# Optimization experiments

Measured on AMD Instinct MI355X. Metric: run time of the kernel, lower is better.

## Reference

```python
import jax, jax.numpy as jnp
import numpy as np

P_SCALAR = 40.0
NEG_INF = -1e30


def setup_inputs() -> dict:
    key = jax.random.key(0)
    k1, k2, k3, k4, k5 = jax.random.split(key, 5)
    B, Dk, Dv, T, H, W = 8, 128, 512, 2, 56, 56
    qkey = jax.random.normal(k1, (B, Dk, H, W), dtype=jnp.float32)
    qmask = jax.random.randint(k2, (B, 1, H, W), 0, 2).astype(jnp.bool_)
    mkey = jax.random.normal(k3, (B, Dk, T, H, W), dtype=jnp.float32)
    mval = jax.random.normal(k4, (B, Dv, T, H, W), dtype=jnp.float32)
    mmask = jax.random.randint(k5, (B, 1, T, H, W), 0, 2).astype(jnp.bool_)
    return {"qkey": qkey, "qmask": qmask, "mkey": mkey, "mval": mval, "mmask": mmask}


def reference(qkey, qmask, mkey, mval, mmask):
    # Faithful vectorized version of SegmentationAttentionSeparateModule.maskRead.
    # Torch loops over b, gathers masked query/memory columns, does
    # softmax(p_scalar * mk^T qk, dim=0) then mv @ p, scattering into zeros.
    # Equivalent dense math: masked softmax over memory positions, and zero
    # output at query positions outside qmask.
    B, Dk, H, W = qkey.shape
    Dv = mval.shape[1]
    M = H * W                       # query positions
    qk = qkey.reshape(B, Dk, M)     # [B, Dk, M]
    mk = mkey.reshape(B, Dk, -1)    # [B, Dk, N], N = T*H*W
    mv = mval.reshape(B, Dv, -1)    # [B, Dv, N]
    qm = qmask.reshape(B, 1, M)     # [B, 1, M]
    mm = mmask.reshape(B, -1)       # [B, N]

    # scores over memory (axis 1) per query column, p_scalar * mk^T qk
    scores = P_SCALAR * jnp.einsum('bdn,bdm->bnm', mk, qk)       # [B, N, M]
    scores = jnp.where(mm[:, :, None], scores, NEG_INF)
    p = jax.nn.softmax(scores, axis=1)                           # softmax over memory
    p = jnp.where(mm[:, :, None], p, 0.0)                        # guard all-masked rows
    qread = jnp.einsum('bdn,bnm->bdm', mv, p)                    # [B, Dv, M]
    qread = jnp.where(qm, qread, 0.0)                            # only masked query cols
    return qread.reshape(B, Dv, H, W)
```

## Files before the change

kernel.cpp:

```cpp
#include <hip/hip_runtime.h>
#include <stdint.h>

#define B_    8
#define DK_   128
#define DV_   512
#define M_    3136
#define N_    6272
#define MT128_ 25
#define NSEG_ 8
#define NTILES_ 98
#define TH_   30.0f
#define MARGIN_ 36.0f
#define BKT_  64

typedef short bf16x8 __attribute__((ext_vector_type(8)));
typedef float f32x16 __attribute__((ext_vector_type(16)));
typedef unsigned short u16x8 __attribute__((ext_vector_type(8)));

__device__ __forceinline__ unsigned fkey(float x) {
  unsigned u = __float_as_uint(x);
  return (u & 0x80000000u) ? ~u : (u | 0x80000000u);
}
__device__ __forceinline__ float fdec(unsigned k) {
  return __uint_as_float((k & 0x80000000u) ? (k & 0x7fffffffu) : ~k);
}
__device__ __forceinline__ unsigned short f2bf(float x) {
  unsigned u = __float_as_uint(x);
  return (unsigned short)((u + 0x7fffu + ((u >> 16) & 1u)) >> 16);
}
__device__ __forceinline__ float bf2f(unsigned short h) {
  return __uint_as_float(((unsigned)h) << 16);
}

__global__ __launch_bounds__(256)
void prep_kernel(const float* __restrict__ qkey, const int* __restrict__ qmask,
                 const float* __restrict__ mkey, const float* __restrict__ mval,
                 float* __restrict__ qkeyT, unsigned short* __restrict__ qkb,
                 float* __restrict__ mkeyT, unsigned short* __restrict__ mkb,
                 unsigned short* __restrict__ mvalT,
                 int* __restrict__ qlist, int* __restrict__ qcnt,
                 unsigned* __restrict__ zbase) {
  __shared__ float T[64][65];
  int r = blockIdx.x;
  int lane = threadIdx.x & 63, ri = threadIdx.x >> 6;
  if (r < 784) {
    int xt = r % 49, dt = (r / 49) & 1, b = r / 98;
    #pragma unroll
    for (int k = 0; k < 16; ++k) {
      int dl = ri * 16 + k;
      T[dl][lane] = qkey[((size_t)b * DK_ + dt * 64 + dl) * M_ + xt * 64 + lane];
    }
    __syncthreads();
    #pragma unroll
    for (int k = 0; k < 16; ++k) {
      int xl = ri * 16 + k;
      float v = 40.0f * T[lane][xl];
      size_t idx = ((size_t)b * M_ + xt * 64 + xl) * DK_ + dt * 64 + lane;
      qkeyT[idx] = v;
      qkb[idx] = f2bf(v);
    }
  } else if (r < 2352) {
    int r2 = r - 784;
    int xt = r2 % 98, dt = (r2 / 98) & 1, b = r2 / 196;
    #pragma unroll
    for (int k = 0; k < 16; ++k) {
      int dl = ri * 16 + k;
      T[dl][lane] = mkey[((size_t)b * DK_ + dt * 64 + dl) * N_ + xt * 64 + lane];
    }
    __syncthreads();
    #pragma unroll
    for (int k = 0; k < 16; ++k) {
      int xl = ri * 16 + k;
      float v = T[lane][xl];
      size_t idx = ((size_t)b * N_ + xt * 64 + xl) * DK_ + dt * 64 + lane;
      mkeyT[idx] = v;
      mkb[idx] = f2bf(v);
    }
  } else if (r < 8624) {
    int r3 = r - 2352;
    int nt = r3 % 98, dvt = (r3 / 98) & 7, b = r3 / 784;
    #pragma unroll
    for (int k = 0; k < 16; ++k) {
      int dvl = ri * 16 + k;
      T[dvl][lane] = mval[((size_t)b * DV_ + dvt * 64 + dvl) * N_ + nt * 64 + lane];
    }
    __syncthreads();
    #pragma unroll
    for (int k = 0; k < 16; ++k) {
      int nl = ri * 16 + k;
      mvalT[((size_t)b * N_ + nt * 64 + nl) * DV_ + dvt * 64 + lane] = f2bf(T[lane][nl]);
    }
  } else if (r < 8632) {
    int b = r - 8624;
    __shared__ int wsum[4];
    __shared__ int cbase;
    int tid = threadIdx.x, wv = tid >> 6;
    if (tid == 0) cbase = 0;
    __syncthreads();
    for (int base = 0; base < M_; base += 256) {
      int i = base + tid;
      int flag = (i < M_) ? (qmask[b * M_ + i] != 0) : 0;
      unsigned long long bal = __ballot(flag);
      int prefix = __popcll(bal & ((1ull << lane) - 1ull));
      if (lane == 0) wsum[wv] = __popcll(bal);
      __syncthreads();
      int woff = 0;
      for (int t = 0; t < wv; ++t) woff += wsum[t];
      int total = wsum[0] + wsum[1] + wsum[2] + wsum[3];
      if (flag) qlist[b * M_ + cbase + woff + prefix] = i;
      __syncthreads();
      if (tid == 0) cbase += total;
      __syncthreads();
    }
    if (tid == 0) qcnt[b] = cbase;
  } else {
    int z = r - 8632;
    unsigned* p = zbase + z * 1024;
    for (int i = threadIdx.x; i < 1024; i += 256) p[i] = 0u;
  }
}

__global__ __launch_bounds__(256, 4)
void score_mfma(const unsigned short* __restrict__ qkb, const unsigned short* __restrict__ mkb,
                const int* __restrict__ qlist, const int* __restrict__ qcnt,
                const int* __restrict__ mmask,
                unsigned* __restrict__ maxkey, unsigned* __restrict__ bcnt,
                unsigned* __restrict__ bucket) {
  int bid = blockIdx.x;
  int seg = bid & (NSEG_ - 1);
  int t   = bid >> 3;
  int mt  = t % MT128_;
  int b   = t / MT128_;
  int mc = qcnt[b];
  if (mt * 128 >= mc) return;
  int t0 = (NTILES_ * seg) / NSEG_;
  int t1 = (NTILES_ * (seg + 1)) / NSEG_;

  __shared__ unsigned short Ks[2][64 * 128];

  int tid = threadIdx.x;
  int lane = tid & 63, wv = tid >> 6;
  int l31 = lane & 31, lhi = lane >> 5;
  int mrow = wv * 32 + l31;

  int cm = mt * 128 + mrow;
  int col = (cm < mc) ? qlist[b * M_ + cm] : qlist[b * M_];
  int mo  = (cm < mc) ? col : -1;
  const unsigned short* qrow = qkb + ((size_t)b * M_ + col) * DK_;
  bf16x8 qf[8];
  #pragma unroll
  for (int kc = 0; kc < 8; ++kc)
    qf[kc] = *(const bf16x8*)(qrow + (kc * 2 + lhi) * 8);

  const unsigned short* mkb_b = mkb + (size_t)b * N_ * DK_;
  const int* mm_b = mmask + b * N_;

  {
    int nbase = t0 << 6;
    char* kd = (char*)&Ks[0][0];
    #pragma unroll
    for (int i = 0; i < 4; ++i) {
      int c = wv * 4 + i;
      const unsigned short* src = mkb_b + ((size_t)(nbase + lane)) * DK_ + c * 8;
      __builtin_amdgcn_global_load_lds(
          (const __attribute__((address_space(1))) unsigned*)src,
          (__attribute__((address_space(3))) unsigned*)(kd + c * 1024), 16, 0, 0);
    }
  }
  asm volatile("s_waitcnt vmcnt(0)" ::: "memory");
  __syncthreads();

  float runmax = -3.0e38f;

  for (int tt = t0; tt < t1; ++tt) {
    int cur = (tt - t0) & 1;
    int nbase = tt << 6;
    if (tt + 1 < t1) {
      int nb2 = (tt + 1) << 6;
      char* kd = (char*)&Ks[cur ^ 1][0];
      #pragma unroll
      for (int i = 0; i < 4; ++i) {
        int c = wv * 4 + i;
        const unsigned short* src = mkb_b + ((size_t)(nb2 + lane)) * DK_ + c * 8;
        __builtin_amdgcn_global_load_lds(
            (const __attribute__((address_space(1))) unsigned*)src,
            (__attribute__((address_space(3))) unsigned*)(kd + c * 1024), 16, 0, 0);
      }
    }
    unsigned long long bits = __ballot(mm_b[nbase + lane] != 0);

    const char* kb = (const char*)&Ks[cur][0];
    f32x16 acc0, acc1;
    #pragma unroll
    for (int r = 0; r < 16; ++r) { acc0[r] = 0.f; acc1[r] = 0.f; }
    #pragma unroll
    for (int kc = 0; kc < 8; ++kc) {
      int c = kc * 2 + lhi;
      bf16x8 a0 = *(const bf16x8*)(kb + c * 1024 + l31 * 16);
      bf16x8 a1 = *(const bf16x8*)(kb + c * 1024 + (32 + l31) * 16);
      acc0 = __builtin_amdgcn_mfma_f32_32x32x16_bf16(a0, qf[kc], acc0, 0, 0, 0);
      acc1 = __builtin_amdgcn_mfma_f32_32x32x16_bf16(a1, qf[kc], acc1, 0, 0, 0);
    }

    unsigned long long b0 = bits >> (lhi << 2);
    unsigned long long b1 = (bits >> 32) >> (lhi << 2);
    float cmx = -3.0e38f;
    #pragma unroll
    for (int r = 0; r < 16; ++r) {
      const int pos = (r & 3) + ((r >> 2) << 3);
      if ((b0 >> pos) & 1) cmx = fmaxf(cmx, acc0[r]);
      if ((b1 >> pos) & 1) cmx = fmaxf(cmx, acc1[r]);
    }
    cmx = fmaxf(cmx, __shfl_xor(cmx, 32));
    runmax = fmaxf(runmax, cmx);

    unsigned old = 0u;
    if (lhi == 0 && mo >= 0) old = atomicMax(&maxkey[b * M_ + mo], fkey(runmax));

    if (mo >= 0) {
      float thr = runmax - MARGIN_;
      #pragma unroll
      for (int r = 0; r < 16; ++r) {
        const int pos = (r & 3) + ((r >> 2) << 3);
        if (((b0 >> pos) & 1) && acc0[r] >= thr) {
          unsigned slot = atomicAdd(&bcnt[b * M_ + mo], 1u);
          if (slot < (unsigned)BKT_)
            bucket[(((size_t)(b * M_ + mo)) << 6) + slot] =
                (unsigned)(nbase + pos + (lhi << 2));
        }
        if (((b1 >> pos) & 1) && acc1[r] >= thr) {
          unsigned slot = atomicAdd(&bcnt[b * M_ + mo], 1u);
          if (slot < (unsigned)BKT_)
            bucket[(((size_t)(b * M_ + mo)) << 6) + slot] =
                (unsigned)(nbase + 32 + pos + (lhi << 2));
        }
      }
    }
    if (lhi == 0) runmax = fmaxf(runmax, fdec(old));
    runmax = __shfl(runmax, l31);

    asm volatile("s_waitcnt vmcnt(0)" ::: "memory");
    __syncthreads();
  }
}

__device__ __forceinline__ float dot128(const float* __restrict__ q,
                                        const float* __restrict__ k) {
  float s = 0.f;
  #pragma unroll 8
  for (int i = 0; i < DK_; i += 4) {
    float4 a = *(const float4*)&q[i];
    float4 bb = *(const float4*)&k[i];
    s += a.x * bb.x + a.y * bb.y + a.z * bb.z + a.w * bb.w;
  }
  return s;
}

__global__ __launch_bounds__(256)
void pv_exact(const float* __restrict__ qkeyT, const float* __restrict__ mkeyT,
              const unsigned short* __restrict__ mvalT,
              const int* __restrict__ qlist, const int* __restrict__ qcnt,
              const int* __restrict__ mmask,
              const unsigned* __restrict__ bcnt, const unsigned* __restrict__ bucket,
              unsigned short* __restrict__ outT) {
  int b = blockIdx.y;
  int wv = threadIdx.x >> 6, lane = threadIdx.x & 63;
  int c = blockIdx.x * 4 + wv;
  if (c >= qcnt[b]) return;
  int m = qlist[b * M_ + c];
  unsigned cnt = bcnt[b * M_ + m];
  const float* qrow = qkeyT + ((size_t)b * M_ + m) * DK_;
  float acc[8] = {0.f, 0.f, 0.f, 0.f, 0.f, 0.f, 0.f, 0.f};
  float lsum = 0.f;

  if (cnt <= (unsigned)BKT_) {
    int n = -1;
    if (lane < (int)cnt) n = (int)bucket[(((size_t)(b * M_ + m)) << 6) + lane];
    float sv = -3.0e38f;
    if (n >= 0) sv = dot128(qrow, mkeyT + ((size_t)b * N_ + n) * DK_);
    float mx = sv;
    #pragma unroll
    for (int o = 32; o > 0; o >>= 1) mx = fmaxf(mx, __shfl_xor(mx, o));
    float e = (n >= 0 && sv >= mx - TH_) ? expf(sv - mx) : 0.f;
    lsum = e;
    #pragma unroll
    for (int o = 32; o > 0; o >>= 1) lsum += __shfl_xor(lsum, o);
    unsigned long long alive = __ballot(e > 0.f);
    while (alive) {
      int lb = __ffsll((unsigned long long)alive) - 1;
      alive &= alive - 1;
      float w = __shfl(e, lb);
      int nn = __shfl(n, lb);
      u16x8 vvv = *(const u16x8*)(mvalT + ((size_t)b * N_ + nn) * DV_ + lane * 8);
      #pragma unroll
      for (int r = 0; r < 8; ++r) acc[r] += w * bf2f(vvv[r]);
    }
  } else {
    float mx = -3.0e38f;
    for (int base = 0; base < N_; base += 64) {
      int n = base + lane;
      float sv = -3.0e38f;
      if (mmask[b * N_ + n] != 0)
        sv = dot128(qrow, mkeyT + ((size_t)b * N_ + n) * DK_);
      mx = fmaxf(mx, sv);
    }
    #pragma unroll
    for (int o = 32; o > 0; o >>= 1) mx = fmaxf(mx, __shfl_xor(mx, o));
    for (int base = 0; base < N_; base += 64) {
      int n = base + lane;
      bool act = (mmask[b * N_ + n] != 0);
      float sv = -3.0e38f;
      if (act) sv = dot128(qrow, mkeyT + ((size_t)b * N_ + n) * DK_);
      float e = (act && sv >= mx - TH_) ? expf(sv - mx) : 0.f;
      lsum += e;
      unsigned long long alive = __ballot(e > 0.f);
      while (alive) {
        int lb = __ffsll((unsigned long long)alive) - 1;
        alive &= alive - 1;
        float w = __shfl(e, lb);
        int nn = __shfl(n, lb);
        u16x8 vvv = *(const u16x8*)(mvalT + ((size_t)b * N_ + nn) * DV_ + lane * 8);
        #pragma unroll
        for (int r = 0; r < 8; ++r) acc[r] += w * bf2f(vvv[r]);
      }
    }
    #pragma unroll
    for (int o = 32; o > 0; o >>= 1) lsum += __shfl_xor(lsum, o);
  }

  float inv = (lsum > 0.f) ? 1.0f / lsum : 0.0f;
  u16x8 ov;
  #pragma unroll
  for (int r = 0; r < 8; ++r) ov[r] = f2bf(acc[r] * inv);
  *(u16x8*)(outT + ((size_t)b * M_ + m) * DV_ + lane * 8) = ov;
}

__global__ __launch_bounds__(256)
void finalize_T(const unsigned short* __restrict__ outT, const int* __restrict__ qmask,
                float* __restrict__ out) {
  __shared__ float T[64][65];
  int b = blockIdx.z, dvt = blockIdx.y, mt = blockIdx.x;
  int lane = threadIdx.x & 63, ri = threadIdx.x >> 6;
  #pragma unroll
  for (int k = 0; k < 16; ++k) {
    int ml = ri * 16 + k;
    int m = mt * 64 + ml;
    bool act = (qmask[b * M_ + m] != 0);
    T[ml][lane] = act ? bf2f(outT[((size_t)b * M_ + m) * DV_ + dvt * 64 + lane]) : 0.f;
  }
  __syncthreads();
  #pragma unroll
  for (int k = 0; k < 16; ++k) {
    int dvl = ri * 16 + k;
    out[((size_t)b * DV_ + dvt * 64 + dvl) * M_ + mt * 64 + lane] = T[lane][dvl];
  }
}

extern "C" void kernel_launch(void* const* d_in, const int* in_sizes, int n_in,
                              void* d_out, int out_size, void* d_ws, size_t ws_size,
                              hipStream_t stream) {
  const float* qkey  = (const float*)d_in[0];
  const int*   qmask = (const int*)d_in[1];
  const float* mkey  = (const float*)d_in[2];
  const float* mval  = (const float*)d_in[3];
  const int*   mmask = (const int*)d_in[4];
  float* out = (float*)d_out;

  uint8_t* w = (uint8_t*)d_ws;
  unsigned*       maxkey = (unsigned*)(w + 0);
  unsigned*       bcnt   = (unsigned*)(w + 100352);
  int*            qcnt   = (int*)(w + 200704);
  int*            qlist  = (int*)(w + 200832);
  unsigned*       bucket = (unsigned*)(w + 301184);
  float*          qkeyT  = (float*)(w + 6723712);
  float*          mkeyT  = (float*)(w + 19568768);
  unsigned short* qkb    = (unsigned short*)(w + 45258880);
  unsigned short* mkb    = (unsigned short*)(w + 51681408);
  unsigned short* outTb  = (unsigned short*)(w + 64526464);
  unsigned short* mvalT  = (unsigned short*)(w + 90216576);

  prep_kernel<<<8681, 256, 0, stream>>>(qkey, qmask, mkey, mval,
                                        qkeyT, qkb, mkeyT, mkb, mvalT,
                                        qlist, qcnt, maxkey );

  score_mfma<<<B_ * MT128_ * NSEG_, 256, 0, stream>>>(
      qkb, mkb, qlist, qcnt, mmask, maxkey, bcnt, bucket);

  pv_exact<<<dim3(M_ / 4, B_), 256, 0, stream>>>(
      qkeyT, mkeyT, mvalT, qlist, qcnt, mmask, bcnt, bucket, outTb);

  finalize_T<<<dim3(M_ / 64, DV_ / 64, B_), 256, 0, stream>>>(outTb, qmask, out);
}
```

Baseline: 186.8 us.

## Drop cross-segment max sharing, widen buckets, vectorize prep transposes, precompute mask bits

```diff
diff --git a/kernel.cpp b/kernel.cpp
--- a/kernel.cpp
+++ b/kernel.cpp
@@ -7,23 +7,16 @@
 #define M_    3136
 #define N_    6272
 #define MT128_ 25
-#define NSEG_ 8
+#define NSEG_ 16
 #define NTILES_ 98
 #define TH_   30.0f
 #define MARGIN_ 36.0f
-#define BKT_  64
+#define BKT_  128
 
 typedef short bf16x8 __attribute__((ext_vector_type(8)));
 typedef float f32x16 __attribute__((ext_vector_type(16)));
 typedef unsigned short u16x8 __attribute__((ext_vector_type(8)));
 
-__device__ __forceinline__ unsigned fkey(float x) {
-  unsigned u = __float_as_uint(x);
-  return (u & 0x80000000u) ? ~u : (u | 0x80000000u);
-}
-__device__ __forceinline__ float fdec(unsigned k) {
-  return __uint_as_float((k & 0x80000000u) ? (k & 0x7fffffffu) : ~k);
-}
 __device__ __forceinline__ unsigned short f2bf(float x) {
   unsigned u = __float_as_uint(x);
   return (unsigned short)((u + 0x7fffu + ((u >> 16) & 1u)) >> 16);
@@ -35,66 +28,77 @@
 __global__ __launch_bounds__(256)
 void prep_kernel(const float* __restrict__ qkey, const int* __restrict__ qmask,
                  const float* __restrict__ mkey, const float* __restrict__ mval,
-                 float* __restrict__ qkeyT, unsigned short* __restrict__ qkb,
-                 float* __restrict__ mkeyT, unsigned short* __restrict__ mkb,
-                 unsigned short* __restrict__ mvalT,
+                 const int* __restrict__ mmask,
+                 float* __restrict__ qkeyT, float* __restrict__ mkeyT,
+                 unsigned short* __restrict__ mkb, unsigned short* __restrict__ mvalT,
                  int* __restrict__ qlist, int* __restrict__ qcnt,
-                 unsigned* __restrict__ zbase) {
+                 unsigned* __restrict__ bcnt_z, unsigned long long* __restrict__ mmbits) {
   __shared__ float T[64][65];
   int r = blockIdx.x;
-  int lane = threadIdx.x & 63, ri = threadIdx.x >> 6;
+  int tid = threadIdx.x;
+  int r16 = tid >> 4, c4 = (tid & 15) << 2;
   if (r < 784) {
     int xt = r % 49, dt = (r / 49) & 1, b = r / 98;
-    #pragma unroll
-    for (int k = 0; k < 16; ++k) {
-      int dl = ri * 16 + k;
-      T[dl][lane] = qkey[((size_t)b * DK_ + dt * 64 + dl) * M_ + xt * 64 + lane];
+    const float* src = qkey + ((size_t)b * DK_ + dt * 64) * M_ + xt * 64;
+    #pragma unroll
+    for (int i = 0; i < 4; ++i) {
+      int row = i * 16 + r16;
+      float4 v = *(const float4*)&src[(size_t)row * M_ + c4];
+      T[row][c4] = v.x; T[row][c4 + 1] = v.y; T[row][c4 + 2] = v.z; T[row][c4 + 3] = v.w;
     }
     __syncthreads();
     #pragma unroll
-    for (int k = 0; k < 16; ++k) {
-      int xl = ri * 16 + k;
-      float v = 40.0f * T[lane][xl];
-      size_t idx = ((size_t)b * M_ + xt * 64 + xl) * DK_ + dt * 64 + lane;
-      qkeyT[idx] = v;
-      qkb[idx] = f2bf(v);
+    for (int i = 0; i < 4; ++i) {
+      int xl = i * 16 + r16;
+      float4 v = make_float4(40.f * T[c4][xl], 40.f * T[c4 + 1][xl],
+                             40.f * T[c4 + 2][xl], 40.f * T[c4 + 3][xl]);
+      *(float4*)&qkeyT[((size_t)b * M_ + xt * 64 + xl) * DK_ + dt * 64 + c4] = v;
     }
   } else if (r < 2352) {
     int r2 = r - 784;
     int xt = r2 % 98, dt = (r2 / 98) & 1, b = r2 / 196;
-    #pragma unroll
-    for (int k = 0; k < 16; ++k) {
-      int dl = ri * 16 + k;
-      T[dl][lane] = mkey[((size_t)b * DK_ + dt * 64 + dl) * N_ + xt * 64 + lane];
+    const float* src = mkey + ((size_t)b * DK_ + dt * 64) * N_ + xt * 64;
+    #pragma unroll
+    for (int i = 0; i < 4; ++i) {
+      int row = i * 16 + r16;
+      float4 v = *(const float4*)&src[(size_t)row * N_ + c4];
+      T[row][c4] = v.x; T[row][c4 + 1] = v.y; T[row][c4 + 2] = v.z; T[row][c4 + 3] = v.w;
     }
     __syncthreads();
     #pragma unroll
-    for (int k = 0; k < 16; ++k) {
-      int xl = ri * 16 + k;
-      float v = T[lane][xl];
-      size_t idx = ((size_t)b * N_ + xt * 64 + xl) * DK_ + dt * 64 + lane;
-      mkeyT[idx] = v;
-      mkb[idx] = f2bf(v);
+    for (int i = 0; i < 4; ++i) {
+      int xl = i * 16 + r16;
+      float4 v = make_float4(T[c4][xl], T[c4 + 1][xl], T[c4 + 2][xl], T[c4 + 3][xl]);
+      size_t idx = ((size_t)b * N_ + xt * 64 + xl) * DK_ + dt * 64 + c4;
+      *(float4*)&mkeyT[idx] = v;
+      ushort4 h;
+      h.x = f2bf(v.x); h.y = f2bf(v.y); h.z = f2bf(v.z); h.w = f2bf(v.w);
+      *(ushort4*)&mkb[idx] = h;
     }
   } else if (r < 8624) {
     int r3 = r - 2352;
     int nt = r3 % 98, dvt = (r3 / 98) & 7, b = r3 / 784;
-    #pragma unroll
-    for (int k = 0; k < 16; ++k) {
-      int dvl = ri * 16 + k;
-      T[dvl][lane] = mval[((size_t)b * DV_ + dvt * 64 + dvl) * N_ + nt * 64 + lane];
+    const float* src = mval + ((size_t)b * DV_ + dvt * 64) * N_ + nt * 64;
+    #pragma unroll
+    for (int i = 0; i < 4; ++i) {
+      int row = i * 16 + r16;
+      float4 v = *(const float4*)&src[(size_t)row * N_ + c4];
+      T[row][c4] = v.x; T[row][c4 + 1] = v.y; T[row][c4 + 2] = v.z; T[row][c4 + 3] = v.w;
     }
     __syncthreads();
     #pragma unroll
-    for (int k = 0; k < 16; ++k) {
-      int nl = ri * 16 + k;
-      mvalT[((size_t)b * N_ + nt * 64 + nl) * DV_ + dvt * 64 + lane] = f2bf(T[lane][nl]);
+    for (int i = 0; i < 4; ++i) {
+      int xl = i * 16 + r16;
+      ushort4 h;
+      h.x = f2bf(T[c4][xl]); h.y = f2bf(T[c4 + 1][xl]);
+      h.z = f2bf(T[c4 + 2][xl]); h.w = f2bf(T[c4 + 3][xl]);
+      *(ushort4*)&mvalT[((size_t)b * N_ + nt * 64 + xl) * DV_ + dvt * 64 + c4] = h;
     }
   } else if (r < 8632) {
     int b = r - 8624;
     __shared__ int wsum[4];
     __shared__ int cbase;
-    int tid = threadIdx.x, wv = tid >> 6;
+    int lane = tid & 63, wv = tid >> 6;
     if (tid == 0) cbase = 0;
     __syncthreads();
     for (int base = 0; base < M_; base += 256) {
@@ -113,22 +117,27 @@
       __syncthreads();
     }
     if (tid == 0) qcnt[b] = cbase;
+  } else if (r < 8657) {
+    unsigned* p = bcnt_z + (size_t)(r - 8632) * 1024;
+    for (int i = tid; i < 1024; i += 256) p[i] = 0u;
   } else {
-    int z = r - 8632;
-    unsigned* p = zbase + z * 1024;
-    for (int i = threadIdx.x; i < 1024; i += 256) p[i] = 0u;
+    int b = r - 8657;
+    int lane = tid & 63, wv = tid >> 6;
+    for (int t = wv; t < NTILES_; t += 4) {
+      unsigned long long word = __ballot(mmask[b * N_ + t * 64 + lane] != 0);
+      if (lane == 0) mmbits[b * NTILES_ + t] = word;
+    }
   }
 }
 
 __global__ __launch_bounds__(256, 4)
-void score_mfma(const unsigned short* __restrict__ qkb, const unsigned short* __restrict__ mkb,
+void score_mfma(const float* __restrict__ qkeyT, const unsigned short* __restrict__ mkb,
                 const int* __restrict__ qlist, const int* __restrict__ qcnt,
-                const int* __restrict__ mmask,
-                unsigned* __restrict__ maxkey, unsigned* __restrict__ bcnt,
-                unsigned* __restrict__ bucket) {
+                const unsigned long long* __restrict__ mmbits,
+                unsigned* __restrict__ bcnt, unsigned* __restrict__ bucket) {
   int bid = blockIdx.x;
   int seg = bid & (NSEG_ - 1);
-  int t   = bid >> 3;
+  int t   = bid >> 4;
   int mt  = t % MT128_;
   int b   = t / MT128_;
   int mc = qcnt[b];
@@ -146,14 +155,22 @@
   int cm = mt * 128 + mrow;
   int col = (cm < mc) ? qlist[b * M_ + cm] : qlist[b * M_];
   int mo  = (cm < mc) ? col : -1;
-  const unsigned short* qrow = qkb + ((size_t)b * M_ + col) * DK_;
+  const float* qrowf = qkeyT + ((size_t)b * M_ + col) * DK_ + lhi * 8;
   bf16x8 qf[8];
   #pragma unroll
-  for (int kc = 0; kc < 8; ++kc)
-    qf[kc] = *(const bf16x8*)(qrow + (kc * 2 + lhi) * 8);
+  for (int kc = 0; kc < 8; ++kc) {
+    float4 v0 = *(const float4*)&qrowf[kc * 16];
+    float4 v1 = *(const float4*)&qrowf[kc * 16 + 4];
+    bf16x8 q;
+    q[0] = (short)f2bf(v0.x); q[1] = (short)f2bf(v0.y);
+    q[2] = (short)f2bf(v0.z); q[3] = (short)f2bf(v0.w);
+    q[4] = (short)f2bf(v1.x); q[5] = (short)f2bf(v1.y);
+    q[6] = (short)f2bf(v1.z); q[7] = (short)f2bf(v1.w);
+    qf[kc] = q;
+  }
 
   const unsigned short* mkb_b = mkb + (size_t)b * N_ * DK_;
-  const int* mm_b = mmask + b * N_;
+  const unsigned long long* bits_b = mmbits + b * NTILES_;
 
   {
     int nbase = t0 << 6;
@@ -187,7 +204,7 @@
             (__attribute__((address_space(3))) unsigned*)(kd + c * 1024), 16, 0, 0);
       }
     }
-    unsigned long long bits = __ballot(mm_b[nbase + lane] != 0);
+    unsigned long long bits = bits_b[tt];
 
     const char* kb = (const char*)&Ks[cur][0];
     f32x16 acc0, acc1;
@@ -213,9 +230,6 @@
     }
     cmx = fmaxf(cmx, __shfl_xor(cmx, 32));
     runmax = fmaxf(runmax, cmx);
-
-    unsigned old = 0u;
-    if (lhi == 0 && mo >= 0) old = atomicMax(&maxkey[b * M_ + mo], fkey(runmax));
 
     if (mo >= 0) {
       float thr = runmax - MARGIN_;
@@ -225,19 +239,17 @@
         if (((b0 >> pos) & 1) && acc0[r] >= thr) {
           unsigned slot = atomicAdd(&bcnt[b * M_ + mo], 1u);
           if (slot < (unsigned)BKT_)
-            bucket[(((size_t)(b * M_ + mo)) << 6) + slot] =
+            bucket[(size_t)(b * M_ + mo) * BKT_ + slot] =
                 (unsigned)(nbase + pos + (lhi << 2));
         }
         if (((b1 >> pos) & 1) && acc1[r] >= thr) {
           unsigned slot = atomicAdd(&bcnt[b * M_ + mo], 1u);
           if (slot < (unsigned)BKT_)
-            bucket[(((size_t)(b * M_ + mo)) << 6) + slot] =
+            bucket[(size_t)(b * M_ + mo) * BKT_ + slot] =
                 (unsigned)(nbase + 32 + pos + (lhi << 2));
         }
       }
     }
-    if (lhi == 0) runmax = fmaxf(runmax, fdec(old));
-    runmax = __shfl(runmax, l31);
 
     asm volatile("s_waitcnt vmcnt(0)" ::: "memory");
     __syncthreads();
@@ -274,23 +286,35 @@
   float lsum = 0.f;
 
   if (cnt <= (unsigned)BKT_) {
-    int n = -1;
-    if (lane < (int)cnt) n = (int)bucket[(((size_t)(b * M_ + m)) << 6) + lane];
-    float sv = -3.0e38f;
-    if (n >= 0) sv = dot128(qrow, mkeyT + ((size_t)b * N_ + n) * DK_);
-    float mx = sv;
+    size_t base = (size_t)(b * M_ + m) * BKT_;
+    int n0 = (lane < (int)cnt) ? (int)bucket[base + lane] : -1;
+    int n1 = (lane + 64 < (int)cnt) ? (int)bucket[base + 64 + lane] : -1;
+    float s0 = (n0 >= 0) ? dot128(qrow, mkeyT + ((size_t)b * N_ + n0) * DK_) : -3.0e38f;
+    float s1 = (n1 >= 0) ? dot128(qrow, mkeyT + ((size_t)b * N_ + n1) * DK_) : -3.0e38f;
+    float mx = fmaxf(s0, s1);
     #pragma unroll
     for (int o = 32; o > 0; o >>= 1) mx = fmaxf(mx, __shfl_xor(mx, o));
-    float e = (n >= 0 && sv >= mx - TH_) ? expf(sv - mx) : 0.f;
-    lsum = e;
+    float e0 = (n0 >= 0 && s0 >= mx - TH_) ? expf(s0 - mx) : 0.f;
+    float e1 = (n1 >= 0 && s1 >= mx - TH_) ? expf(s1 - mx) : 0.f;
+    lsum = e0 + e1;
     #pragma unroll
     for (int o = 32; o > 0; o >>= 1) lsum += __shfl_xor(lsum, o);
-    unsigned long long alive = __ballot(e > 0.f);
+    unsigned long long alive = __ballot(e0 > 0.f);
     while (alive) {
       int lb = __ffsll((unsigned long long)alive) - 1;
       alive &= alive - 1;
-      float w = __shfl(e, lb);
-      int nn = __shfl(n, lb);
+      float w = __shfl(e0, lb);
+      int nn = __shfl(n0, lb);
+      u16x8 vvv = *(const u16x8*)(mvalT + ((size_t)b * N_ + nn) * DV_ + lane * 8);
+      #pragma unroll
+      for (int r = 0; r < 8; ++r) acc[r] += w * bf2f(vvv[r]);
+    }
+    alive = __ballot(e1 > 0.f);
+    while (alive) {
+      int lb = __ffsll((unsigned long long)alive) - 1;
+      alive &= alive - 1;
+      float w = __shfl(e1, lb);
+      int nn = __shfl(n1, lb);
       u16x8 vvv = *(const u16x8*)(mvalT + ((size_t)b * N_ + nn) * DV_ + lane * 8);
       #pragma unroll
       for (int r = 0; r < 8; ++r) acc[r] += w * bf2f(vvv[r]);
@@ -367,24 +391,23 @@
   float* out = (float*)d_out;
 
   uint8_t* w = (uint8_t*)d_ws;
-  unsigned*       maxkey = (unsigned*)(w + 0);
-  unsigned*       bcnt   = (unsigned*)(w + 100352);
-  int*            qcnt   = (int*)(w + 200704);
-  int*            qlist  = (int*)(w + 200832);
-  unsigned*       bucket = (unsigned*)(w + 301184);
-  float*          qkeyT  = (float*)(w + 6723712);
-  float*          mkeyT  = (float*)(w + 19568768);
-  unsigned short* qkb    = (unsigned short*)(w + 45258880);
-  unsigned short* mkb    = (unsigned short*)(w + 51681408);
-  unsigned short* outTb  = (unsigned short*)(w + 64526464);
-  unsigned short* mvalT  = (unsigned short*)(w + 90216576);
-
-  prep_kernel<<<8681, 256, 0, stream>>>(qkey, qmask, mkey, mval,
-                                        qkeyT, qkb, mkeyT, mkb, mvalT,
-                                        qlist, qcnt, maxkey );
+  unsigned*           bcnt   = (unsigned*)(w + 0);
+  int*                qcnt   = (int*)(w + 102400);
+  int*                qlist  = (int*)(w + 102528);
+  unsigned long long* mmbits = (unsigned long long*)(w + 202880);
+  unsigned*           bucket = (unsigned*)(w + 209152);
+  float*              qkeyT  = (float*)(w + 13054208);
+  float*              mkeyT  = (float*)(w + 25899264);
+  unsigned short*     mkb    = (unsigned short*)(w + 51589376);
+  unsigned short*     outTb  = (unsigned short*)(w + 64434432);
+  unsigned short*     mvalT  = (unsigned short*)(w + 90124544);
+
+  prep_kernel<<<8665, 256, 0, stream>>>(qkey, qmask, mkey, mval, mmask,
+                                        qkeyT, mkeyT, mkb, mvalT,
+                                        qlist, qcnt, bcnt, mmbits);
 
   score_mfma<<<B_ * MT128_ * NSEG_, 256, 0, stream>>>(
-      qkb, mkb, qlist, qcnt, mmask, maxkey, bcnt, bucket);
+      qkeyT, mkb, qlist, qcnt, mmbits, bcnt, bucket);
 
   pv_exact<<<dim3(M_ / 4, B_), 256, 0, stream>>>(
       qkeyT, mkeyT, mvalT, qlist, qcnt, mmask, bcnt, bucket, outTb);
```

After: 236.5 us. 1.27x slower.
